# Kernel tuning notes

Hardware: AMD Instinct MI355X
Metric: run time of the kernel (lower is better)

## Reference

```python
import jax, jax.numpy as jnp
import numpy as np

N_NODES = 100000
N_EDGES = 1600000
N_FEAT = 128
N_GRAPHS = 256
N_CLASSES = 2
BN_EPS = 1e-5


def _glorot(key, shape):
    lim = float(np.sqrt(6.0 / (shape[0] + shape[1])))
    return jax.random.uniform(key, shape, jnp.float32, -lim, lim)


def setup_inputs() -> dict:
    key = jax.random.key(0)
    ks = jax.random.split(key, 16)
    x = jax.random.normal(ks[0], (N_NODES, N_FEAT), jnp.float32)
    edge_index = jax.random.randint(ks[1], (2, N_EDGES), 0, N_NODES, jnp.int64)
    batch = jnp.sort(jax.random.randint(ks[2], (N_NODES,), 0, N_GRAPHS, jnp.int64))
    dims = [(N_FEAT, 16), (16, 32), (32, 64), (64, 50)]
    params = {}
    for i, (di, do) in enumerate(dims):
        params[f"W{i+1}"] = _glorot(ks[3 + i], (di, do))
        params[f"b{i+1}"] = jnp.zeros((do,), jnp.float32)
    params["bn_gamma"] = jnp.ones((50,), jnp.float32)
    params["bn_beta"] = jnp.zeros((50,), jnp.float32)
    params["fc1_W"] = _glorot(ks[8], (50, 30))
    params["fc1_b"] = jnp.zeros((30,), jnp.float32)
    params["fc2_W"] = _glorot(ks[9], (30, 20))
    params["fc2_b"] = jnp.zeros((20,), jnp.float32)
    params["fc3_W"] = _glorot(ks[10], (20, N_CLASSES))
    params["fc3_b"] = jnp.zeros((N_CLASSES,), jnp.float32)
    return {"x": x, "edge_index": edge_index, "batch": batch, **params}


def _gcn(x, W, b, src, dst):
    # GCNConv with normalize=False: out_i = sum_{(j->i) in E} (x_j @ W) + b
    h = x @ W                                   # [N, d_out]
    agg = jax.ops.segment_sum(h[src], dst, num_segments=N_NODES)
    return agg + b


def reference(x, edge_index, batch,
              W1, b1, W2, b2, W3, b3, W4, b4,
              bn_gamma, bn_beta,
              fc1_W, fc1_b, fc2_W, fc2_b, fc3_W, fc3_b):
    src, dst = edge_index[0], edge_index[1]
    lrelu = lambda v: jax.nn.leaky_relu(v, 0.01)
    h = lrelu(_gcn(x, W1, b1, src, dst))
    h = lrelu(_gcn(h, W2, b2, src, dst))
    h = lrelu(_gcn(h, W3, b3, src, dst))
    h = _gcn(h, W4, b4, src, dst)
    # BatchNorm over the node dimension (training-style batch stats, biased var)
    mu = jnp.mean(h, axis=0)
    var = jnp.mean((h - mu) ** 2, axis=0)
    h = lrelu((h - mu) * jax.lax.rsqrt(var + BN_EPS) * bn_gamma + bn_beta)
    # global_add_pool over graphs
    g = jax.ops.segment_sum(h, batch, num_segments=N_GRAPHS)   # [G, 50]
    g = lrelu(g @ fc1_W + fc1_b)   # dropout inactive (eval)
    g = lrelu(g @ fc2_W + fc2_b)
    g = g @ fc3_W + fc3_b
    return jax.nn.log_softmax(g, axis=-1)
```

## Files before the change

### kernel.cpp

```cpp
#include <hip/hip_runtime.h>

#define N_NODES 100000
#define N_EDGES 1600000
#define N_GRAPHS 256
#define NBKT 196
#define BKT_CAP 16384
#define BCHUNKS 391
#define MM1_BLOCKS 3125
#define A_BLOCKS (BCHUNKS + MM1_BLOCKS)

__device__ __forceinline__ float lrelu(float v) { return v > 0.f ? v : 0.01f * v; }

__device__ __forceinline__ unsigned short f2bf(float f) {
    unsigned int u = __float_as_uint(f);
    return (unsigned short)((u + 0x7FFFu + ((u >> 16) & 1u)) >> 16);
}
__device__ __forceinline__ float bf2f(unsigned short h) {
    return __uint_as_float(((unsigned int)h) << 16);
}
__device__ __forceinline__ float blo(unsigned int v) { return __uint_as_float(v << 16); }
__device__ __forceinline__ float bhi(unsigned int v) { return __uint_as_float(v & 0xFFFF0000u); }

__global__ void bucket_and_mm1(const int* __restrict__ src, const int* __restrict__ dst,
                               int* __restrict__ bucketCnt, unsigned int* __restrict__ bkt,
                               const float* __restrict__ x, const float* __restrict__ W1,
                               unsigned short* __restrict__ T1) {
    __shared__ float lds[32 * 132 + 128 * 16];
    int bid = blockIdx.x;
    int tid = threadIdx.x;
    if (bid % 9 == 0) {
        int* lcnt = (int*)lds;
        int* loff = lcnt + 784;
        int* lcnt2 = loff + 784;
        int fi = bid / 9;
        for (int i = tid; i < 784; i += 256) { lcnt[i] = 0; lcnt2[i] = 0; }
        __syncthreads();
        int sub = tid & 3;
        int e0 = fi * 4096 + tid;
#pragma unroll
        for (int i = 0; i < 16; ++i) {
            int e = e0 + i * 256;
            if (e < N_EDGES) {
                int b = dst[e] >> 9;
                atomicAdd(&lcnt[sub * 196 + b], 1);
            }
        }
        __syncthreads();
        if (tid < NBKT) {
            int c0 = lcnt[tid], c1 = lcnt[196 + tid], c2 = lcnt[392 + tid], c3 = lcnt[588 + tid];
            int tot = c0 + c1 + c2 + c3;
            int goff = (tot > 0) ? atomicAdd(&bucketCnt[tid], tot) : 0;
            loff[tid] = goff;
            loff[196 + tid] = goff + c0;
            loff[392 + tid] = goff + c0 + c1;
            loff[588 + tid] = goff + c0 + c1 + c2;
        }
        __syncthreads();
#pragma unroll
        for (int i = 0; i < 16; ++i) {
            int e = e0 + i * 256;
            if (e < N_EDGES) {
                int d = dst[e];
                int s = src[e];
                int b = d >> 9;
                int pos = loff[sub * 196 + b] + atomicAdd(&lcnt2[sub * 196 + b], 1);
                if (pos < BKT_CAP)
                    bkt[(size_t)b * BKT_CAP + pos] =
                        ((unsigned int)(d & 511) << 17) | (unsigned int)s;
            }
        }
    } else {
        int mb = bid - bid / 9 - 1;
        float* xs = lds;
        float* wsm = lds + 32 * 132;
        const int n0 = mb * 32;
        for (int i = tid; i < 128 * 16; i += 256) wsm[i] = W1[i];
        const float4* X4 = (const float4*)x;
        for (int i = tid; i < 32 * 32; i += 256) {
            int r2 = i >> 5, c = i & 31;
            ((float4*)(xs + r2 * 132))[c] = X4[(size_t)(n0 + r2) * 32 + c];
        }
        __syncthreads();
        int r2 = tid >> 3, jp = tid & 7;
        float a0 = 0.f, a1 = 0.f;
        const float* xr = xs + r2 * 132;
#pragma unroll
        for (int k = 0; k < 128; ++k) {
            float2 wv = *(const float2*)(wsm + k * 16 + 2 * jp);
            float xv = xr[k];
            a0 = fmaf(xv, wv.x, a0);
            a1 = fmaf(xv, wv.y, a1);
        }
        ((unsigned int*)T1)[(size_t)(n0 + r2) * 8 + jp] = ((unsigned int)f2bf(a1) << 16) | f2bf(a0);
    }
}

__global__ void build_bucket(const unsigned int* __restrict__ bkt, const int* __restrict__ bucketCnt,
                             int* __restrict__ base, int* __restrict__ adj) {
    __shared__ int ldeg[512];
    __shared__ int lofs[512];
    __shared__ int ssum[256];
    int b = blockIdx.x;
    int tid = threadIdx.x;
    ssum[tid] = (tid < NBKT) ? bucketCnt[tid] : 0;
    __syncthreads();
    for (int off = 1; off < 256; off <<= 1) {
        int add = (tid >= off) ? ssum[tid - off] : 0;
        __syncthreads();
        ssum[tid] += add;
        __syncthreads();
    }
    int gbase = (b > 0) ? ssum[b - 1] : 0;
    int cnt = min(((b < NBKT) ? bucketCnt[b] : 0), BKT_CAP);
    int nstart = b * 512;
    int nn = min(512, N_NODES - nstart);
    const unsigned int* seg = bkt + (size_t)b * BKT_CAP;
    for (int i = tid; i < 512; i += 256) ldeg[i] = 0;
    __syncthreads();
    for (int e = tid; e < cnt; e += 256) atomicAdd(&ldeg[seg[e] >> 17], 1);
    __syncthreads();
    int a0 = ldeg[2 * tid], a1 = ldeg[2 * tid + 1];
    __syncthreads();
    ssum[tid] = a0 + a1;
    __syncthreads();
    for (int off = 1; off < 256; off <<= 1) {
        int add = (tid >= off) ? ssum[tid - off] : 0;
        __syncthreads();
        ssum[tid] += add;
        __syncthreads();
    }
    int prev = (tid > 0) ? ssum[tid - 1] : 0;
    lofs[2 * tid] = prev;
    lofs[2 * tid + 1] = prev + a0;
    __syncthreads();
    for (int i = tid; i < nn; i += 256) base[nstart + i] = gbase + lofs[i];
    if (b == 0 && tid == 0) base[N_NODES] = N_EDGES;
    for (int i = tid; i < 512; i += 256) ldeg[i] = 0;
    __syncthreads();
    for (int e = tid; e < cnt; e += 256) {
        unsigned int v = seg[e];
        int dl = (int)(v >> 17);
        int pos = atomicAdd(&ldeg[dl], 1);
        adj[gbase + lofs[dl] + pos] = (int)(v & 0x1FFFFu);
    }
}

template <int DIN, int DOUT, int ROWS, bool BIAS, bool RELU>
__global__ void matmul_rt(const unsigned int* __restrict__ X2, const float* __restrict__ W,
                          unsigned short* __restrict__ T, const float* __restrict__ bias) {
    constexpr int PAIRS = DOUT / 2;
    constexpr int PT = (PAIRS + 3) / 4;
    constexpr int RT = ROWS / 4;
    constexpr int XST = DIN + 1;
    __shared__ float xs[ROWS * XST];
    __shared__ float wsm[DIN * DOUT + 8];
    const int n0 = blockIdx.x * ROWS;
    const bool full = (n0 + ROWS <= N_NODES);
    int tid = threadIdx.x;
    for (int i = tid; i < DIN * DOUT; i += 256) wsm[i] = W[i];
    constexpr int V = DIN / 2;
    for (int i = tid; i < ROWS * V; i += 256) {
        int r = i / V, c = i - r * V;
        int node = n0 + r;
        unsigned int v = (full || node < N_NODES) ? X2[(size_t)node * V + c] : 0u;
        xs[r * XST + 2 * c]     = blo(v);
        xs[r * XST + 2 * c + 1] = bhi(v);
    }
    __syncthreads();
    if (tid >= RT * PT) return;
    int rt = tid / PT, pt = tid - rt * PT;
    const float* xr0 = xs + (rt * 4) * XST;
    const float* wp = wsm + 2 * (pt * 4);
    float2 acc[4][4];
#pragma unroll
    for (int i = 0; i < 4; ++i)
#pragma unroll
        for (int j = 0; j < 4; ++j) acc[i][j] = make_float2(0.f, 0.f);
#pragma unroll 4
    for (int k = 0; k < DIN; ++k) {
        float xv0 = xr0[k];
        float xv1 = xr0[XST + k];
        float xv2 = xr0[2 * XST + k];
        float xv3 = xr0[3 * XST + k];
        const float* wr = wp + k * DOUT;
        float2 w0 = *(const float2*)(wr);
        float2 w1 = *(const float2*)(wr + 2);
        float2 w2 = *(const float2*)(wr + 4);
        float2 w3 = *(const float2*)(wr + 6);
        acc[0][0].x = fmaf(xv0, w0.x, acc[0][0].x); acc[0][0].y = fmaf(xv0, w0.y, acc[0][0].y);
        acc[0][1].x = fmaf(xv0, w1.x, acc[0][1].x); acc[0][1].y = fmaf(xv0, w1.y, acc[0][1].y);
        acc[0][2].x = fmaf(xv0, w2.x, acc[0][2].x); acc[0][2].y = fmaf(xv0, w2.y, acc[0][2].y);
        acc[0][3].x = fmaf(xv0, w3.x, acc[0][3].x); acc[0][3].y = fmaf(xv0, w3.y, acc[0][3].y);
        acc[1][0].x = fmaf(xv1, w0.x, acc[1][0].x); acc[1][0].y = fmaf(xv1, w0.y, acc[1][0].y);
        acc[1][1].x = fmaf(xv1, w1.x, acc[1][1].x); acc[1][1].y = fmaf(xv1, w1.y, acc[1][1].y);
        acc[1][2].x = fmaf(xv1, w2.x, acc[1][2].x); acc[1][2].y = fmaf(xv1, w2.y, acc[1][2].y);
        acc[1][3].x = fmaf(xv1, w3.x, acc[1][3].x); acc[1][3].y = fmaf(xv1, w3.y, acc[1][3].y);
        acc[2][0].x = fmaf(xv2, w0.x, acc[2][0].x); acc[2][0].y = fmaf(xv2, w0.y, acc[2][0].y);
        acc[2][1].x = fmaf(xv2, w1.x, acc[2][1].x); acc[2][1].y = fmaf(xv2, w1.y, acc[2][1].y);
        acc[2][2].x = fmaf(xv2, w2.x, acc[2][2].x); acc[2][2].y = fmaf(xv2, w2.y, acc[2][2].y);
        acc[2][3].x = fmaf(xv2, w3.x, acc[2][3].x); acc[2][3].y = fmaf(xv2, w3.y, acc[2][3].y);
        acc[3][0].x = fmaf(xv3, w0.x, acc[3][0].x); acc[3][0].y = fmaf(xv3, w0.y, acc[3][0].y);
        acc[3][1].x = fmaf(xv3, w1.x, acc[3][1].x); acc[3][1].y = fmaf(xv3, w1.y, acc[3][1].y);
        acc[3][2].x = fmaf(xv3, w2.x, acc[3][2].x); acc[3][2].y = fmaf(xv3, w2.y, acc[3][2].y);
        acc[3][3].x = fmaf(xv3, w3.x, acc[3][3].x); acc[3][3].y = fmaf(xv3, w3.y, acc[3][3].y);
    }
    unsigned int* Tu = (unsigned int*)T;
#pragma unroll
    for (int i = 0; i < 4; ++i) {
        int node = n0 + rt * 4 + i;
        if (full || node < N_NODES) {
#pragma unroll
            for (int j = 0; j < 4; ++j) {
                int jp = pt * 4 + j;
                if (PAIRS % 4 == 0 || jp < PAIRS) {
                    float a0 = acc[i][j].x, a1 = acc[i][j].y;
                    if (BIAS) { a0 += bias[2 * jp]; a1 += bias[2 * jp + 1]; }
                    if (RELU) { a0 = lrelu(a0); a1 = lrelu(a1); }
                    Tu[(size_t)node * PAIRS + jp] = ((unsigned int)f2bf(a1) << 16) | f2bf(a0);
                }
            }
        }
    }
}

template <int DOUT, bool BIAS, bool RELU>
__global__ void gather_agg_bf16(const unsigned short* __restrict__ T, const int* __restrict__ base,
                                const int* __restrict__ adj, const float* __restrict__ b,
                                unsigned short* __restrict__ out) {
    constexpr int PAIRS = DOUT / 2;
    int gi = blockIdx.x * 256 + threadIdx.x;
    int node = gi / PAIRS;
    int j = gi - node * PAIRS;
    if (node >= N_NODES) return;
    const unsigned int* Tu = (const unsigned int*)T;
    int e0 = base[node], e1 = base[node + 1];
    float a0 = 0.f, a1 = 0.f, c0 = 0.f, c1 = 0.f;
    int k = e0;
    for (; k + 3 < e1; k += 4) {
        int s0 = adj[k], s1 = adj[k + 1], s2 = adj[k + 2], s3 = adj[k + 3];
        unsigned int v0 = Tu[(size_t)s0 * PAIRS + j];
        unsigned int v1 = Tu[(size_t)s1 * PAIRS + j];
        unsigned int v2 = Tu[(size_t)s2 * PAIRS + j];
        unsigned int v3 = Tu[(size_t)s3 * PAIRS + j];
        a0 += blo(v0); a1 += bhi(v0);
        c0 += blo(v1); c1 += bhi(v1);
        a0 += blo(v2); a1 += bhi(v2);
        c0 += blo(v3); c1 += bhi(v3);
    }
    for (; k < e1; ++k) {
        int s = adj[k];
        unsigned int v = Tu[(size_t)s * PAIRS + j];
        a0 += blo(v); a1 += bhi(v);
    }
    a0 += c0; a1 += c1;
    if (BIAS) { a0 += b[2 * j]; a1 += b[2 * j + 1]; }
    if (RELU) { a0 = lrelu(a0); a1 = lrelu(a1); }
    ((unsigned int*)out)[(size_t)node * PAIRS + j] = ((unsigned int)f2bf(a1) << 16) | f2bf(a0);
}

__global__ void bn_partial_kernel(const unsigned short* __restrict__ H, float* __restrict__ sum,
                                  float* __restrict__ ssum) {
    int tid = threadIdx.x;
    int j = tid % 50;
    int sub = tid / 50;
    float s = 0.f, ss = 0.f;
    if (tid < 250) {
        for (int node = blockIdx.x * 5 + sub; node < N_NODES; node += gridDim.x * 5) {
            float v = bf2f(H[(size_t)node * 50 + j]);
            s += v;
            ss += v * v;
        }
    }
    __shared__ float ls[256], lss[256];
    ls[tid] = s;
    lss[tid] = ss;
    __syncthreads();
    if (tid < 50) {
        float a = ls[tid] + ls[tid + 50] + ls[tid + 100] + ls[tid + 150] + ls[tid + 200];
        float c = lss[tid] + lss[tid + 50] + lss[tid + 100] + lss[tid + 150] + lss[tid + 200];
        atomicAdd(&sum[tid], a);
        atomicAdd(&ssum[tid], c);
    }
}

__global__ void find_bounds_kernel(const int* __restrict__ batch, int* __restrict__ bounds) {
    int g = blockIdx.x * blockDim.x + threadIdx.x;
    if (g > N_GRAPHS) return;
    int lo = 0, hi = N_NODES;
    while (lo < hi) {
        int mid = (lo + hi) >> 1;
        if (batch[mid] < g) lo = mid + 1; else hi = mid;
    }
    bounds[g] = lo;
}

__global__ void pool_seg_kernel(const unsigned short* __restrict__ H, const int* __restrict__ bounds,
                                const float* __restrict__ bnsum, const float* __restrict__ bnssum,
                                const float* __restrict__ gamma, const float* __restrict__ beta,
                                float* __restrict__ G) {
    int g = blockIdx.x;
    int s = bounds[g], e = bounds[g + 1];
    int tid = threadIdx.x;
    int j = tid % 50;
    int sub = tid / 50;
    float acc = 0.f;
    if (tid < 250) {
        float m = bnsum[j] / (float)N_NODES;
        float var = bnssum[j] / (float)N_NODES - m * m;
        float rs = rsqrtf(fmaxf(var, 0.f) + 1e-5f);
        float scale = rs * gamma[j];
        float shift = beta[j] - m * scale;
        for (int n = s + sub; n < e; n += 5) {
            float v = fmaf(bf2f(H[(size_t)n * 50 + j]), scale, shift);
            acc += lrelu(v);
        }
    }
    __shared__ float ls[256];
    ls[tid] = acc;
    __syncthreads();
    if (tid < 50) {
        G[g * 50 + tid] = ls[tid] + ls[tid + 50] + ls[tid + 100] + ls[tid + 150] + ls[tid + 200];
    }
}

__global__ void mlp_kernel(const float* __restrict__ G,
                           const float* __restrict__ fc1W, const float* __restrict__ fc1b,
                           const float* __restrict__ fc2W, const float* __restrict__ fc2b,
                           const float* __restrict__ fc3W, const float* __restrict__ fc3b,
                           float* __restrict__ out) {
    __shared__ float lw[2192];
    int tid = threadIdx.x;
    for (int i = tid; i < 1500; i += 256) lw[i] = fc1W[i];
    for (int i = tid; i < 30; i += 256) lw[1500 + i] = fc1b[i];
    for (int i = tid; i < 600; i += 256) lw[1530 + i] = fc2W[i];
    for (int i = tid; i < 20; i += 256) lw[2130 + i] = fc2b[i];
    for (int i = tid; i < 40; i += 256) lw[2150 + i] = fc3W[i];
    for (int i = tid; i < 2; i += 256) lw[2190 + i] = fc3b[i];
    __syncthreads();
    int g = blockIdx.x * 32 + tid;
    if (tid >= 32 || g >= N_GRAPHS) return;
    float a[50];
#pragma unroll
    for (int k = 0; k < 50; ++k) a[k] = G[g * 50 + k];
    float h1[30];
#pragma unroll
    for (int j = 0; j < 30; ++j) {
        float acc = lw[1500 + j];
#pragma unroll
        for (int k = 0; k < 50; ++k) acc = fmaf(a[k], lw[k * 30 + j], acc);
        h1[j] = lrelu(acc);
    }
    float h2[20];
#pragma unroll
    for (int j = 0; j < 20; ++j) {
        float acc = lw[2130 + j];
#pragma unroll
        for (int k = 0; k < 30; ++k) acc = fmaf(h1[k], lw[1530 + k * 20 + j], acc);
        h2[j] = lrelu(acc);
    }
    float z0 = lw[2190], z1 = lw[2191];
#pragma unroll
    for (int k = 0; k < 20; ++k) {
        z0 = fmaf(h2[k], lw[2150 + k * 2 + 0], z0);
        z1 = fmaf(h2[k], lw[2150 + k * 2 + 1], z1);
    }
    float m = fmaxf(z0, z1);
    float lse = m + logf(expf(z0 - m) + expf(z1 - m));
    out[g * 2 + 0] = z0 - lse;
    out[g * 2 + 1] = z1 - lse;
}

extern "C" void kernel_launch(void* const* d_in, const int* in_sizes, int n_in,
                              void* d_out, int out_size, void* d_ws, size_t ws_size,
                              hipStream_t stream) {
    const float* x     = (const float*)d_in[0];
    const int*   ei    = (const int*)d_in[1];
    const int*   batch = (const int*)d_in[2];
    const float* W1 = (const float*)d_in[3];  const float* b1 = (const float*)d_in[4];
    const float* W2 = (const float*)d_in[5];  const float* b2 = (const float*)d_in[6];
    const float* W3 = (const float*)d_in[7];  const float* b3 = (const float*)d_in[8];
    const float* W4 = (const float*)d_in[9];  const float* b4 = (const float*)d_in[10];
    const float* bng = (const float*)d_in[11]; const float* bnb = (const float*)d_in[12];
    const float* fc1W = (const float*)d_in[13]; const float* fc1b = (const float*)d_in[14];
    const float* fc2W = (const float*)d_in[15]; const float* fc2b = (const float*)d_in[16];
    const float* fc3W = (const float*)d_in[17]; const float* fc3b = (const float*)d_in[18];

    const int* src = ei;
    const int* dst = ei + N_EDGES;

    char* w = (char*)d_ws;
    unsigned short* bufA = (unsigned short*)w;      w += (size_t)6400000 * 2;
    unsigned short* bufB = (unsigned short*)w;      w += (size_t)6400000 * 2;
    int*   adj  = (int*)w;                          w += (size_t)N_EDGES * 4;
    unsigned int* bkt = (unsigned int*)w;           w += (size_t)NBKT * BKT_CAP * 4;
    int*   base = (int*)w;                          w += (size_t)(N_NODES + 1) * 4;
    int*   bucketCnt = (int*)w;                     w += 256 * 4;
    float* bnsum = (float*)w;                       w += 64 * 4;
    float* bnssum = (float*)w;                      w += 64 * 4;
    int*   bounds = (int*)w;                        w += (N_GRAPHS + 1) * 4;
    float* G    = (float*)w;                        w += (size_t)N_GRAPHS * 50 * 4;

    dim3 blk(256);

    hipMemsetAsync(bucketCnt, 0, 256 * 4, stream);
    find_bounds_kernel<<<2, 256, 0, stream>>>(batch, bounds);

    bucket_and_mm1<<<A_BLOCKS, blk, 0, stream>>>(src, dst, bucketCnt, bkt, x, W1, bufA);

    build_bucket<<<NBKT, blk, 0, stream>>>(bkt, bucketCnt, base, adj);

    gather_agg_bf16<16, true, true><<<(N_NODES * 8 + 255) / 256, blk, 0, stream>>>(bufA, base, adj, b1, bufB);

    gather_agg_bf16<16, false, false><<<(N_NODES * 8 + 255) / 256, blk, 0, stream>>>(bufB, base, adj, nullptr, bufA);
    matmul_rt<16, 32, 256, true, true><<<(N_NODES + 255) / 256, blk, 0, stream>>>((const unsigned int*)bufA, W2, bufB, b2);

    gather_agg_bf16<32, false, false><<<(N_NODES * 16 + 255) / 256, blk, 0, stream>>>(bufB, base, adj, nullptr, bufA);
    matmul_rt<32, 64, 128, true, true><<<(N_NODES + 127) / 128, blk, 0, stream>>>((const unsigned int*)bufA, W3, bufB, b3);

    matmul_rt<64, 50, 128, false, false><<<(N_NODES + 127) / 128, blk, 0, stream>>>((const unsigned int*)bufB, W4, bufA, nullptr);
    gather_agg_bf16<50, true, false><<<(N_NODES * 25 + 255) / 256, blk, 0, stream>>>(bufA, base, adj, b4, bufB);

    hipMemsetAsync(bnsum, 0, 128 * 4, stream);
    bn_partial_kernel<<<256, blk, 0, stream>>>(bufB, bnsum, bnssum);

    pool_seg_kernel<<<N_GRAPHS, blk, 0, stream>>>(bufB, bounds, bnsum, bnssum, bng, bnb, G);

    mlp_kernel<<<8, 256, 0, stream>>>(G, fc1W, fc1b, fc2W, fc2b, fc3W, fc3b, (float*)d_out);
}
```

Baseline: 311.4 us.

## Cache edge indices in registers, vectorize mm1 loads, unroll gather by 8, fuse memsets

The bucketing pass now keeps dst/src values in registers from the counting pass and reuses them in the scatter pass instead of reading global memory twice. The mm1 inner loop reads x from LDS as float4. The gather loop gains an 8-wide unrolled stage so more independent loads are in flight per thread. The two memsets are folded into the bounds kernel, which cuts two launches. The main costs are higher register pressure from the 16-entry caches and the wider unroll.

```diff
diff --git a/kernel.cpp b/kernel.cpp
--- a/kernel.cpp
+++ b/kernel.cpp
@@ -37,12 +37,14 @@
         __syncthreads();
         int sub = tid & 3;
         int e0 = fi * 4096 + tid;
+        int dcache[16], scache[16];
 #pragma unroll
         for (int i = 0; i < 16; ++i) {
             int e = e0 + i * 256;
             if (e < N_EDGES) {
-                int b = dst[e] >> 9;
-                atomicAdd(&lcnt[sub * 196 + b], 1);
+                dcache[i] = dst[e];
+                scache[i] = src[e];
+                atomicAdd(&lcnt[sub * 196 + (dcache[i] >> 9)], 1);
             }
         }
         __syncthreads();
@@ -60,13 +62,12 @@
         for (int i = 0; i < 16; ++i) {
             int e = e0 + i * 256;
             if (e < N_EDGES) {
-                int d = dst[e];
-                int s = src[e];
+                int d = dcache[i];
                 int b = d >> 9;
                 int pos = loff[sub * 196 + b] + atomicAdd(&lcnt2[sub * 196 + b], 1);
                 if (pos < BKT_CAP)
                     bkt[(size_t)b * BKT_CAP + pos] =
-                        ((unsigned int)(d & 511) << 17) | (unsigned int)s;
+                        ((unsigned int)(d & 511) << 17) | (unsigned int)scache[i];
             }
         }
     } else {
@@ -83,13 +84,18 @@
         __syncthreads();
         int r2 = tid >> 3, jp = tid & 7;
         float a0 = 0.f, a1 = 0.f;
-        const float* xr = xs + r2 * 132;
-#pragma unroll
-        for (int k = 0; k < 128; ++k) {
-            float2 wv = *(const float2*)(wsm + k * 16 + 2 * jp);
-            float xv = xr[k];
-            a0 = fmaf(xv, wv.x, a0);
-            a1 = fmaf(xv, wv.y, a1);
+        const float4* xr4 = (const float4*)(xs + r2 * 132);
+#pragma unroll
+        for (int k4 = 0; k4 < 32; ++k4) {
+            float4 xv = xr4[k4];
+            float2 w0 = *(const float2*)(wsm + (4 * k4 + 0) * 16 + 2 * jp);
+            float2 w1 = *(const float2*)(wsm + (4 * k4 + 1) * 16 + 2 * jp);
+            float2 w2 = *(const float2*)(wsm + (4 * k4 + 2) * 16 + 2 * jp);
+            float2 w3 = *(const float2*)(wsm + (4 * k4 + 3) * 16 + 2 * jp);
+            a0 = fmaf(xv.x, w0.x, a0); a1 = fmaf(xv.x, w0.y, a1);
+            a0 = fmaf(xv.y, w1.x, a0); a1 = fmaf(xv.y, w1.y, a1);
+            a0 = fmaf(xv.z, w2.x, a0); a1 = fmaf(xv.z, w2.y, a1);
+            a0 = fmaf(xv.w, w3.x, a0); a1 = fmaf(xv.w, w3.y, a1);
         }
         ((unsigned int*)T1)[(size_t)(n0 + r2) * 8 + jp] = ((unsigned int)f2bf(a1) << 16) | f2bf(a0);
     }
@@ -236,6 +242,26 @@
     int e0 = base[node], e1 = base[node + 1];
     float a0 = 0.f, a1 = 0.f, c0 = 0.f, c1 = 0.f;
     int k = e0;
+    for (; k + 7 < e1; k += 8) {
+        int s0 = adj[k], s1 = adj[k + 1], s2 = adj[k + 2], s3 = adj[k + 3];
+        int s4 = adj[k + 4], s5 = adj[k + 5], s6 = adj[k + 6], s7 = adj[k + 7];
+        unsigned int v0 = Tu[(size_t)s0 * PAIRS + j];
+        unsigned int v1 = Tu[(size_t)s1 * PAIRS + j];
+        unsigned int v2 = Tu[(size_t)s2 * PAIRS + j];
+        unsigned int v3 = Tu[(size_t)s3 * PAIRS + j];
+        unsigned int v4 = Tu[(size_t)s4 * PAIRS + j];
+        unsigned int v5 = Tu[(size_t)s5 * PAIRS + j];
+        unsigned int v6 = Tu[(size_t)s6 * PAIRS + j];
+        unsigned int v7 = Tu[(size_t)s7 * PAIRS + j];
+        a0 += blo(v0); a1 += bhi(v0);
+        c0 += blo(v1); c1 += bhi(v1);
+        a0 += blo(v2); a1 += bhi(v2);
+        c0 += blo(v3); c1 += bhi(v3);
+        a0 += blo(v4); a1 += bhi(v4);
+        c0 += blo(v5); c1 += bhi(v5);
+        a0 += blo(v6); a1 += bhi(v6);
+        c0 += blo(v7); c1 += bhi(v7);
+    }
     for (; k + 3 < e1; k += 4) {
         int s0 = adj[k], s1 = adj[k + 1], s2 = adj[k + 2], s3 = adj[k + 3];
         unsigned int v0 = Tu[(size_t)s0 * PAIRS + j];
@@ -283,8 +309,17 @@
     }
 }
 
-__global__ void find_bounds_kernel(const int* __restrict__ batch, int* __restrict__ bounds) {
-    int g = blockIdx.x * blockDim.x + threadIdx.x;
+__global__ void setup_kernel(const int* __restrict__ batch, int* __restrict__ bounds,
+                             int* __restrict__ bucketCnt, float* __restrict__ bnsum,
+                             float* __restrict__ bnssum) {
+    int tid = threadIdx.x;
+    if (blockIdx.x == 0) {
+        bucketCnt[tid] = 0;
+    } else if (tid < 64) {
+        bnsum[tid] = 0.f;
+        bnssum[tid] = 0.f;
+    }
+    int g = blockIdx.x * 256 + tid;
     if (g > N_GRAPHS) return;
     int lo = 0, hi = N_NODES;
     while (lo < hi) {
@@ -402,8 +437,7 @@
 
     dim3 blk(256);
 
-    hipMemsetAsync(bucketCnt, 0, 256 * 4, stream);
-    find_bounds_kernel<<<2, 256, 0, stream>>>(batch, bounds);
+    setup_kernel<<<2, 256, 0, stream>>>(batch, bounds, bucketCnt, bnsum, bnssum);
 
     bucket_and_mm1<<<A_BLOCKS, blk, 0, stream>>>(src, dst, bucketCnt, bkt, x, W1, bufA);
 
@@ -420,7 +454,6 @@
     matmul_rt<64, 50, 128, false, false><<<(N_NODES + 127) / 128, blk, 0, stream>>>((const unsigned int*)bufB, W4, bufA, nullptr);
     gather_agg_bf16<50, true, false><<<(N_NODES * 25 + 255) / 256, blk, 0, stream>>>(bufA, base, adj, b4, bufB);
 
-    hipMemsetAsync(bnsum, 0, 128 * 4, stream);
     bn_partial_kernel<<<256, blk, 0, stream>>>(bufB, bnsum, bnssum);
 
     pool_seg_kernel<<<N_GRAPHS, blk, 0, stream>>>(bufB, bounds, bnsum, bnssum, bng, bnb, G);
```

Result: faster. 282.3 us (median of 2 runs) (-9.3%).
